# Kernel tuning notes

Measured on AMD Instinct MI355X. Metric: run time of the kernel, lower is better.

Reference implementation:

```python
import jax, jax.numpy as jnp
import numpy as np

CAPACITY = 0.5  # top_k = int(seq_len * capacity)

def setup_inputs() -> dict:
    key = jax.random.key(0)
    k1, k2, k3, k4 = jax.random.split(key, 4)
    b, s, d, d_ff = 4, 4096, 1024, 4096
    x = jax.random.normal(k1, (b, s, d), dtype=jnp.float32)
    mask = jnp.ones((b, s), dtype=jnp.bool_)
    # learned params: router (Linear(d,1,bias=False)) and the block MLP
    Wr = jax.random.normal(k2, (d, 1), dtype=jnp.float32) * (d ** -0.5)
    W1 = jax.random.normal(k3, (d, d_ff), dtype=jnp.float32) * (d ** -0.5)
    W2 = jax.random.normal(k4, (d_ff, d), dtype=jnp.float32) * (d_ff ** -0.5)
    return {"x": x, "mask": mask, "Wr": Wr, "W1": W1, "W2": W2}

def reference(x, mask, Wr, W1, W2):
    b, s, d = x.shape
    top_k = int(s * CAPACITY)
    # router logits [b, s]
    logits = (x @ Wr)[..., 0]
    # top-k over sequence dim (torch sorted=False; softmax/gather are
    # permutation-equivariant so sorted top_k gives identical results)
    vals, idx = jax.lax.top_k(logits, top_k)          # [b, k]
    order = jnp.argsort(idx, axis=1)                  # sort selected indices ascending
    sel = jnp.take_along_axis(idx, order, axis=1)     # [b, k] token positions, ascending
    w = jax.nn.softmax(vals, axis=1)                  # softmax over selected logits
    r_w = jnp.take_along_axis(w, order, axis=1)       # weights reordered to match sel
    # gather selected tokens
    fx = jnp.take_along_axis(x, sel[..., None], axis=1)  # [b, k, d]
    # block: residual MLP whose update is scaled by router weights (mask unused by MLP)
    h = jax.nn.silu(fx @ W1) @ W2
    out = fx + h * r_w[..., None]
    # scatter processed tokens back into x
    batch = jnp.arange(b)[:, None]
    hidden_states = x.at[batch, sel].set(out)
    # aux loss: faithful to the original (flat view + flat index set, then BCE-with-logits mean)
    flat_logits = logits.reshape(-1)                  # [b*s]
    targets = jnp.zeros_like(flat_logits).at[sel.reshape(-1)].set(1.0)
    aux_loss = jnp.mean(
        jnp.maximum(flat_logits, 0.0)
        - flat_logits * targets
        + jnp.log1p(jnp.exp(-jnp.abs(flat_logits)))
    )
    return hidden_states, aux_loss
```

## Files before the change

kernel.cpp:

```cpp
#include <hip/hip_runtime.h>
#include <hip/hip_bf16.h>
#include <cstdint>

#define B_ 4
#define S_ 4096
#define D_ 1024
#define DFF_ 4096
#define KSEL_ 2048
#define M_ (B_ * KSEL_)
#define NTOK_ (B_ * S_)

typedef short bf16x8 __attribute__((ext_vector_type(8)));
typedef float f32x4 __attribute__((ext_vector_type(4)));

__device__ inline unsigned short f2bf(float f) {
    union { float f; unsigned int u; } c; c.f = f;
    unsigned int u = c.u;
    unsigned int r = u + 0x7fffu + ((u >> 16) & 1u);
    return (unsigned short)(r >> 16);
}

__global__ __launch_bounds__(256)
void transpose_both(const float* __restrict__ W1, unsigned short* __restrict__ W1T,
                    const float* __restrict__ W2, unsigned short* __restrict__ W2T) {
    __shared__ float tile[32][33];
    const float* src; unsigned short* dst; int R, C, c0, r0;
    if (blockIdx.z == 0) { src = W1; dst = W1T; R = D_;  C = DFF_;
                           c0 = blockIdx.x * 32; r0 = blockIdx.y * 32; }
    else                 { src = W2; dst = W2T; R = DFF_; C = D_;
                           c0 = blockIdx.y * 32; r0 = blockIdx.x * 32; }
    for (int i = threadIdx.y; i < 32; i += 8)
        tile[i][threadIdx.x] = src[(size_t)(r0 + i) * C + c0 + threadIdx.x];
    __syncthreads();
    for (int i = threadIdx.y; i < 32; i += 8)
        dst[(size_t)(c0 + i) * R + r0 + threadIdx.x] = f2bf(tile[threadIdx.x][i]);
}

__global__ __launch_bounds__(256)
void router_kernel(const float* __restrict__ x, const float* __restrict__ Wr,
                   float* __restrict__ logits, unsigned short* __restrict__ xb,
                   float* __restrict__ out) {
    int wid = threadIdx.x >> 6, lane = threadIdx.x & 63;
    int row = blockIdx.x * 4 + wid;
    const float* xr = x + (size_t)row * D_;
    unsigned short* xbr = xb + (size_t)row * D_;
    float* outr = out + (size_t)row * D_;
    float acc = 0.f;
#pragma unroll
    for (int j = 0; j < 4; j++) {
        int off = j * 256 + lane * 4;
        float4 v = *(const float4*)(xr + off);
        float4 w = *(const float4*)(Wr + off);
        acc += v.x * w.x + v.y * w.y + v.z * w.z + v.w * w.w;
        *(float4*)(outr + off) = v;
        ushort4 o;
        o.x = f2bf(v.x); o.y = f2bf(v.y); o.z = f2bf(v.z); o.w = f2bf(v.w);
        *(ushort4*)(xbr + off) = o;
    }
#pragma unroll
    for (int s = 32; s; s >>= 1) acc += __shfl_xor(acc, s);
    if (lane == 0) logits[row] = acc;
}

__global__ __launch_bounds__(256)
void rank_partial_kernel(const float* __restrict__ logits, int* __restrict__ rank) {
    __shared__ float lj[512];
    int b  = blockIdx.x >> 7;
    int ic = (blockIdx.x >> 3) & 15;
    int jc = blockIdx.x & 7;
    const float* L = logits + b * S_;
    for (int t = threadIdx.x; t < 512; t += 256) lj[t] = L[jc * 512 + t];
    __syncthreads();
    int i = ic * 256 + threadIdx.x;
    float li = L[i];
    int jbase = jc * 512;
    int r = 0;
    const float4* __restrict__ lj4 = (const float4*)lj;
#pragma unroll 4
    for (int q = 0; q < 128; q++) {
        float4 v = lj4[q];
        int jb = jbase + q * 4;
        r += (v.x > li) | ((v.x == li) & (jb     < i));
        r += (v.y > li) | ((v.y == li) & (jb + 1 < i));
        r += (v.z > li) | ((v.z == li) & (jb + 2 < i));
        r += (v.w > li) | ((v.w == li) & (jb + 3 < i));
    }
    atomicAdd(&rank[b * S_ + i], r);
}

__global__ __launch_bounds__(256)
void compact_kernel(const float* __restrict__ logits, const int* __restrict__ rank,
                    int* __restrict__ rowidx, float* __restrict__ rw) {
    __shared__ float lg[S_];
    __shared__ int f[S_];
    __shared__ int tsum[256];
    __shared__ float red[256];
    int b = blockIdx.x;
    const float* L = logits + b * S_;
    const int* R = rank + b * S_;
    for (int j = threadIdx.x; j < S_ / 4; j += 256) {
        ((float4*)lg)[j] = ((const float4*)L)[j];
        int4 rk = ((const int4*)R)[j];
        int4 fl;
        fl.x = rk.x < KSEL_; fl.y = rk.y < KSEL_;
        fl.z = rk.z < KSEL_; fl.w = rk.w < KSEL_;
        ((int4*)f)[j] = fl;
    }
    __syncthreads();
    float mx = -INFINITY;
    for (int j = threadIdx.x; j < S_; j += 256) mx = fmaxf(mx, lg[j]);
    red[threadIdx.x] = mx; __syncthreads();
    for (int s = 128; s; s >>= 1) {
        if (threadIdx.x < s) red[threadIdx.x] = fmaxf(red[threadIdx.x], red[threadIdx.x + s]);
        __syncthreads();
    }
    float m = red[0];
    __syncthreads();

    float esum = 0.f;
    int s0 = 0;
#pragma unroll
    for (int j = 0; j < 16; j++) {
        int i = threadIdx.x * 16 + j;
        s0 += f[i];
        if (f[i]) esum += expf(lg[i] - m);
    }
    red[threadIdx.x] = esum; __syncthreads();
    for (int s = 128; s; s >>= 1) {
        if (threadIdx.x < s) red[threadIdx.x] += red[threadIdx.x + s];
        __syncthreads();
    }
    float inv = 1.f / red[0];

    tsum[threadIdx.x] = s0; __syncthreads();
    for (int s = 1; s < 256; s <<= 1) {
        int u = (threadIdx.x >= s) ? tsum[threadIdx.x - s] : 0;
        __syncthreads();
        tsum[threadIdx.x] += u;
        __syncthreads();
    }
    int pos = tsum[threadIdx.x] - s0;
    for (int j = 0; j < 16; j++) {
        int i = threadIdx.x * 16 + j;
        if (f[i]) {
            rowidx[b * KSEL_ + pos] = b * S_ + i;
            rw[b * KSEL_ + pos] = expf(lg[i] - m) * inv;
            pos++;
        }
    }
}

__global__ __launch_bounds__(256)
void loss_kernel(const float* __restrict__ logits, const int* __restrict__ rank,
                 float* __restrict__ partials) {
    __shared__ float red[256];
    int i = blockIdx.x * 256 + threadIdx.x;
    float l = logits[i];
    float t = 0.f;
    if (i < S_)
        t = ((rank[i] < KSEL_) | (rank[S_ + i] < KSEL_) |
             (rank[2 * S_ + i] < KSEL_) | (rank[3 * S_ + i] < KSEL_)) ? 1.f : 0.f;
    float v = fmaxf(l, 0.f) - l * t + log1pf(expf(-fabsf(l)));
    red[threadIdx.x] = v; __syncthreads();
    for (int s = 128; s; s >>= 1) {
        if (threadIdx.x < s) red[threadIdx.x] += red[threadIdx.x + s];
        __syncthreads();
    }
    if (threadIdx.x == 0) partials[blockIdx.x] = red[0];
}

__global__ void loss_final(const float* __restrict__ partials, float* __restrict__ out) {
    float v = partials[threadIdx.x];
#pragma unroll
    for (int s = 32; s; s >>= 1) v += __shfl_xor(v, s);
    if (threadIdx.x == 0) out[0] = v / (float)NTOK_;
}

template <int MODE>
__global__ __launch_bounds__(256)
void gemm_bt_kernel(const unsigned short* __restrict__ A,
                    const unsigned short* __restrict__ BT,
                    const int* __restrict__ rowidx,
                    const float* __restrict__ rw,
                    const float* __restrict__ x,
                    unsigned short* __restrict__ Hout,
                    float* __restrict__ Out,
                    int K, int N) {
    __shared__ __attribute__((aligned(16))) unsigned short As[128 * 64];
    __shared__ __attribute__((aligned(16))) unsigned short Bs[128 * 64];
    __shared__ __attribute__((aligned(16))) float Cs[32 * 132];
    const int tid = threadIdx.x;
    const int w = tid >> 6, lane = tid & 63;
    const int wm = w >> 1, wn = w & 1;
    const int tile_m = blockIdx.x * 128;
    const int tile_n = blockIdx.y * 128;

    const int srow = lane >> 3;
    const int sw = (lane & 7) ^ srow;
    const uint64_t abase = (uint64_t)(uintptr_t)A;
    const uint64_t bbase = (uint64_t)(uintptr_t)BT;
    uint64_t aaddr[4], baddr[4];
#pragma unroll
    for (int t = 0; t < 4; ++t) {
        int r = t * 32 + w * 8 + srow;
        int am = tile_m + r;
        int ar = (MODE == 1) ? rowidx[am] : am;
        aaddr[t] = abase + ((uint64_t)ar * K + (uint64_t)sw * 8) * 2ull;
        int bn = tile_n + r;
        baddr[t] = bbase + ((uint64_t)bn * K + (uint64_t)sw * 8) * 2ull;
    }

    f32x4 acc[4][4];
#pragma unroll
    for (int i = 0; i < 4; i++)
#pragma unroll
        for (int j = 0; j < 4; j++) acc[i][j] = (f32x4){0.f, 0.f, 0.f, 0.f};

    const int lr = lane & 15, quad = lane >> 4;
    const int KI = K >> 6;
    for (int it = 0; it < KI; ++it) {
        const uint64_t koff = (uint64_t)(it * 64) * 2ull;
#pragma unroll
        for (int t = 0; t < 4; ++t) {
            unsigned short* ldsA = &As[(t * 32 + w * 8) * 64];
            unsigned short* ldsB = &Bs[(t * 32 + w * 8) * 64];
            __builtin_amdgcn_global_load_lds(
                (const __attribute__((address_space(1))) unsigned int*)(uintptr_t)(aaddr[t] + koff),
                (__attribute__((address_space(3))) unsigned int*)ldsA, 16, 0, 0);
            __builtin_amdgcn_global_load_lds(
                (const __attribute__((address_space(1))) unsigned int*)(uintptr_t)(baddr[t] + koff),
                (__attribute__((address_space(3))) unsigned int*)ldsB, 16, 0, 0);
        }
        __syncthreads();
#pragma unroll
        for (int ks = 0; ks < 2; ++ks) {
            bf16x8 af[4], bfr[4];
#pragma unroll
            for (int t4 = 0; t4 < 4; ++t4) {
                int row = wm * 64 + t4 * 16 + lr;
                int kc = ks * 4 + quad;
                af[t4] = *(const bf16x8*)((const char*)As + row * 128 + ((kc ^ (lr & 7)) * 16));
                int nr = wn * 64 + t4 * 16 + lr;
                bfr[t4] = *(const bf16x8*)((const char*)Bs + nr * 128 + ((kc ^ (lr & 7)) * 16));
            }
#pragma unroll
            for (int ti = 0; ti < 4; ++ti)
#pragma unroll
                for (int tj = 0; tj < 4; ++tj)
                    acc[ti][tj] = __builtin_amdgcn_mfma_f32_16x16x32_bf16(
                        af[ti], bfr[tj], acc[ti][tj], 0, 0, 0);
        }
        __syncthreads();
    }

    const int erow = tid >> 3;
    const int eseg = tid & 7;
#pragma unroll
    for (int p = 0; p < 4; ++p) {
        if (p) __syncthreads();
        if (wm == (p >> 1)) {
#pragma unroll
            for (int t = 0; t < 2; ++t) {
                int ti = (p & 1) * 2 + t;
#pragma unroll
                for (int tj = 0; tj < 4; ++tj) {
                    int rbase = t * 16 + quad * 4;
                    int col = wn * 64 + tj * 16 + lr;
#pragma unroll
                    for (int r = 0; r < 4; ++r)
                        Cs[(rbase + r) * 132 + col] = acc[ti][tj][r];
                }
            }
        }
        __syncthreads();
        int m = tile_m + p * 32 + erow;
        const float* crow = Cs + erow * 132 + eseg * 16;
        if (MODE == 1) {
            uint64_t hb = (uint64_t)m * N + tile_n + eseg * 16;
#pragma unroll
            for (int c = 0; c < 2; ++c) {
                f32x4 v0 = *(const f32x4*)(crow + c * 8);
                f32x4 v1 = *(const f32x4*)(crow + c * 8 + 4);
                float s[8];
#pragma unroll
                for (int j = 0; j < 4; ++j) {
                    s[j]     = v0[j] * __builtin_amdgcn_rcpf(1.f + __expf(-v0[j]));
                    s[4 + j] = v1[j] * __builtin_amdgcn_rcpf(1.f + __expf(-v1[j]));
                }
                union { __hip_bfloat162 h; unsigned int u; } cv;
                uint4 pk;
                cv.h = __float22bfloat162_rn(float2{s[0], s[1]}); pk.x = cv.u;
                cv.h = __float22bfloat162_rn(float2{s[2], s[3]}); pk.y = cv.u;
                cv.h = __float22bfloat162_rn(float2{s[4], s[5]}); pk.z = cv.u;
                cv.h = __float22bfloat162_rn(float2{s[6], s[7]}); pk.w = cv.u;
                *(uint4*)(Hout + hb + c * 8) = pk;
            }
        } else {
            int grow = rowidx[m];
            float wgt = rw[m];
            uint64_t gb = (uint64_t)grow * D_ + tile_n + eseg * 16;
#pragma unroll
            for (int c = 0; c < 4; ++c) {
                f32x4 v = *(const f32x4*)(crow + c * 4);
                float4 xv = *(const float4*)(x + gb + c * 4);
                float4 o;
                o.x = xv.x + v[0] * wgt;
                o.y = xv.y + v[1] * wgt;
                o.z = xv.z + v[2] * wgt;
                o.w = xv.w + v[3] * wgt;
                *(float4*)(Out + gb + c * 4) = o;
            }
        }
    }
}

extern "C" void kernel_launch(void* const* d_in, const int* in_sizes, int n_in,
                              void* d_out, int out_size, void* d_ws, size_t ws_size,
                              hipStream_t stream) {
    const float* x  = (const float*)d_in[0];
    const float* Wr = (const float*)d_in[2];
    const float* W1 = (const float*)d_in[3];
    const float* W2 = (const float*)d_in[4];
    float* out = (float*)d_out;

    char* ws = (char*)d_ws;
    size_t off = 0;
    auto alloc = [&](size_t bytes) {
        char* p = ws + off;
        off = (off + bytes + 255) & ~(size_t)255;
        return p;
    };
    unsigned short* xb   = (unsigned short*)alloc((size_t)NTOK_ * D_ * 2);
    unsigned short* W1bT = (unsigned short*)alloc((size_t)DFF_ * D_ * 2);
    unsigned short* W2bT = (unsigned short*)alloc((size_t)D_ * DFF_ * 2);
    unsigned short* H    = (unsigned short*)alloc((size_t)M_ * DFF_ * 2);
    float* logits  = (float*)alloc(NTOK_ * 4);
    int*   rank    = (int*)alloc(NTOK_ * 4);
    int*   rowidx  = (int*)alloc(M_ * 4);
    float* rwp     = (float*)alloc(M_ * 4);
    float* partials = (float*)alloc(64 * 4);

    (void)hipMemsetAsync(rank, 0, NTOK_ * 4, stream);

    transpose_both<<<dim3(128, 32, 2), dim3(32, 8), 0, stream>>>(W1, W1bT, W2, W2bT);
    router_kernel<<<NTOK_ / 4, 256, 0, stream>>>(x, Wr, logits, xb, out);
    rank_partial_kernel<<<512, 256, 0, stream>>>(logits, rank);
    compact_kernel<<<B_, 256, 0, stream>>>(logits, rank, rowidx, rwp);
    loss_kernel<<<NTOK_ / 256, 256, 0, stream>>>(logits, rank, partials);
    loss_final<<<1, 64, 0, stream>>>(partials, out + (size_t)NTOK_ * D_);
    gemm_bt_kernel<1><<<dim3(M_ / 128, DFF_ / 128), 256, 0, stream>>>(
        xb, W1bT, rowidx, nullptr, nullptr, H, nullptr, D_, DFF_);
    gemm_bt_kernel<2><<<dim3(M_ / 128, D_ / 128), 256, 0, stream>>>(
        H, W2bT, rowidx, rwp, x, nullptr, out, DFF_, D_);
}
```

Baseline: 372.0 us.

## Split GEMM kernels, use 64-row tiles for second GEMM, copy only unselected rows

The templated GEMM is split into two kernels. The second GEMM now uses 64x128 tiles, which doubles its block count from 512 to 1024 so more CUs stay busy on the small N=1024 output. The router kernel no longer writes all of x to the output. A new kernel copies only the unselected rows after ranking, which halves the redundant output write traffic. The cost is an extra kernel launch and less operand reuse per block in the second GEMM.

```diff
diff --git a/kernel.cpp b/kernel.cpp
--- a/kernel.cpp
+++ b/kernel.cpp
@@ -38,13 +38,11 @@
 
 __global__ __launch_bounds__(256)
 void router_kernel(const float* __restrict__ x, const float* __restrict__ Wr,
-                   float* __restrict__ logits, unsigned short* __restrict__ xb,
-                   float* __restrict__ out) {
+                   float* __restrict__ logits, unsigned short* __restrict__ xb) {
     int wid = threadIdx.x >> 6, lane = threadIdx.x & 63;
     int row = blockIdx.x * 4 + wid;
     const float* xr = x + (size_t)row * D_;
     unsigned short* xbr = xb + (size_t)row * D_;
-    float* outr = out + (size_t)row * D_;
     float acc = 0.f;
 #pragma unroll
     for (int j = 0; j < 4; j++) {
@@ -52,7 +50,6 @@
         float4 v = *(const float4*)(xr + off);
         float4 w = *(const float4*)(Wr + off);
         acc += v.x * w.x + v.y * w.y + v.z * w.z + v.w * w.w;
-        *(float4*)(outr + off) = v;
         ushort4 o;
         o.x = f2bf(v.x); o.y = f2bf(v.y); o.z = f2bf(v.z); o.w = f2bf(v.w);
         *(ushort4*)(xbr + off) = o;
@@ -89,6 +86,16 @@
 }
 
 __global__ __launch_bounds__(256)
+void copy_unselected_kernel(const float* __restrict__ x, const int* __restrict__ rank,
+                            float* __restrict__ out) {
+    int row = blockIdx.x;
+    if (rank[row] < KSEL_) return;
+    const float4* src = (const float4*)(x + (size_t)row * D_);
+    float4* dst = (float4*)(out + (size_t)row * D_);
+    dst[threadIdx.x] = src[threadIdx.x];
+}
+
+__global__ __launch_bounds__(256)
 void compact_kernel(const float* __restrict__ logits, const int* __restrict__ rank,
                     int* __restrict__ rowidx, float* __restrict__ rw) {
     __shared__ float lg[S_];
@@ -176,16 +183,12 @@
     if (threadIdx.x == 0) out[0] = v / (float)NTOK_;
 }
 
-template <int MODE>
-__global__ __launch_bounds__(256)
-void gemm_bt_kernel(const unsigned short* __restrict__ A,
-                    const unsigned short* __restrict__ BT,
-                    const int* __restrict__ rowidx,
-                    const float* __restrict__ rw,
-                    const float* __restrict__ x,
-                    unsigned short* __restrict__ Hout,
-                    float* __restrict__ Out,
-                    int K, int N) {
+__global__ __launch_bounds__(256)
+void gemm1_kernel(const unsigned short* __restrict__ A,
+                  const unsigned short* __restrict__ BT,
+                  const int* __restrict__ rowidx,
+                  unsigned short* __restrict__ Hout,
+                  int K, int N) {
     __shared__ __attribute__((aligned(16))) unsigned short As[128 * 64];
     __shared__ __attribute__((aligned(16))) unsigned short Bs[128 * 64];
     __shared__ __attribute__((aligned(16))) float Cs[32 * 132];
@@ -203,8 +206,7 @@
 #pragma unroll
     for (int t = 0; t < 4; ++t) {
         int r = t * 32 + w * 8 + srow;
-        int am = tile_m + r;
-        int ar = (MODE == 1) ? rowidx[am] : am;
+        int ar = rowidx[tile_m + r];
         aaddr[t] = abase + ((uint64_t)ar * K + (uint64_t)sw * 8) * 2ull;
         int bn = tile_n + r;
         baddr[t] = bbase + ((uint64_t)bn * K + (uint64_t)sw * 8) * 2ull;
@@ -253,8 +255,7 @@
         __syncthreads();
     }
 
-    const int erow = tid >> 3;
-    const int eseg = tid & 7;
+    const int erow = tid >> 3, eseg = tid & 7;
 #pragma unroll
     for (int p = 0; p < 4; ++p) {
         if (p) __syncthreads();
@@ -275,41 +276,137 @@
         __syncthreads();
         int m = tile_m + p * 32 + erow;
         const float* crow = Cs + erow * 132 + eseg * 16;
-        if (MODE == 1) {
-            uint64_t hb = (uint64_t)m * N + tile_n + eseg * 16;
-#pragma unroll
-            for (int c = 0; c < 2; ++c) {
-                f32x4 v0 = *(const f32x4*)(crow + c * 8);
-                f32x4 v1 = *(const f32x4*)(crow + c * 8 + 4);
-                float s[8];
-#pragma unroll
-                for (int j = 0; j < 4; ++j) {
-                    s[j]     = v0[j] * __builtin_amdgcn_rcpf(1.f + __expf(-v0[j]));
-                    s[4 + j] = v1[j] * __builtin_amdgcn_rcpf(1.f + __expf(-v1[j]));
-                }
-                union { __hip_bfloat162 h; unsigned int u; } cv;
-                uint4 pk;
-                cv.h = __float22bfloat162_rn(float2{s[0], s[1]}); pk.x = cv.u;
-                cv.h = __float22bfloat162_rn(float2{s[2], s[3]}); pk.y = cv.u;
-                cv.h = __float22bfloat162_rn(float2{s[4], s[5]}); pk.z = cv.u;
-                cv.h = __float22bfloat162_rn(float2{s[6], s[7]}); pk.w = cv.u;
-                *(uint4*)(Hout + hb + c * 8) = pk;
+        uint64_t hb = (uint64_t)m * N + tile_n + eseg * 16;
+#pragma unroll
+        for (int c = 0; c < 2; ++c) {
+            f32x4 v0 = *(const f32x4*)(crow + c * 8);
+            f32x4 v1 = *(const f32x4*)(crow + c * 8 + 4);
+            float s[8];
+#pragma unroll
+            for (int j = 0; j < 4; ++j) {
+                s[j]     = v0[j] * __builtin_amdgcn_rcpf(1.f + __expf(-v0[j]));
+                s[4 + j] = v1[j] * __builtin_amdgcn_rcpf(1.f + __expf(-v1[j]));
             }
-        } else {
-            int grow = rowidx[m];
-            float wgt = rw[m];
-            uint64_t gb = (uint64_t)grow * D_ + tile_n + eseg * 16;
-#pragma unroll
-            for (int c = 0; c < 4; ++c) {
-                f32x4 v = *(const f32x4*)(crow + c * 4);
-                float4 xv = *(const float4*)(x + gb + c * 4);
-                float4 o;
-                o.x = xv.x + v[0] * wgt;
-                o.y = xv.y + v[1] * wgt;
-                o.z = xv.z + v[2] * wgt;
-                o.w = xv.w + v[3] * wgt;
-                *(float4*)(Out + gb + c * 4) = o;
+            union { __hip_bfloat162 h; unsigned int u; } cv;
+            uint4 pk;
+            cv.h = __float22bfloat162_rn(float2{s[0], s[1]}); pk.x = cv.u;
+            cv.h = __float22bfloat162_rn(float2{s[2], s[3]}); pk.y = cv.u;
+            cv.h = __float22bfloat162_rn(float2{s[4], s[5]}); pk.z = cv.u;
+            cv.h = __float22bfloat162_rn(float2{s[6], s[7]}); pk.w = cv.u;
+            *(uint4*)(Hout + hb + c * 8) = pk;
+        }
+    }
+}
+
+__global__ __launch_bounds__(256)
+void gemm2_kernel(const unsigned short* __restrict__ A,
+                  const unsigned short* __restrict__ BT,
+                  const int* __restrict__ rowidx,
+                  const float* __restrict__ rw,
+                  const float* __restrict__ x,
+                  float* __restrict__ Out,
+                  int K, int N) {
+    __shared__ __attribute__((aligned(16))) unsigned short As[64 * 64];
+    __shared__ __attribute__((aligned(16))) unsigned short Bs[128 * 64];
+    __shared__ __attribute__((aligned(16))) float Cs[16 * 132];
+    const int tid = threadIdx.x;
+    const int w = tid >> 6, lane = tid & 63;
+    const int tile_m = blockIdx.x * 64;
+    const int tile_n = blockIdx.y * 128;
+
+    const int srow = lane >> 3;
+    const int sw = (lane & 7) ^ srow;
+    const uint64_t abase = (uint64_t)(uintptr_t)A;
+    const uint64_t bbase = (uint64_t)(uintptr_t)BT;
+    uint64_t aaddr[2], baddr[4];
+#pragma unroll
+    for (int t = 0; t < 2; ++t) {
+        int r = t * 32 + w * 8 + srow;
+        aaddr[t] = abase + ((uint64_t)(tile_m + r) * K + (uint64_t)sw * 8) * 2ull;
+    }
+#pragma unroll
+    for (int t = 0; t < 4; ++t) {
+        int bn = tile_n + t * 32 + w * 8 + srow;
+        baddr[t] = bbase + ((uint64_t)bn * K + (uint64_t)sw * 8) * 2ull;
+    }
+
+    f32x4 acc[4][2];
+#pragma unroll
+    for (int i = 0; i < 4; i++)
+#pragma unroll
+        for (int j = 0; j < 2; j++) acc[i][j] = (f32x4){0.f, 0.f, 0.f, 0.f};
+
+    const int lr = lane & 15, quad = lane >> 4;
+    const int KI = K >> 6;
+    for (int it = 0; it < KI; ++it) {
+        const uint64_t koff = (uint64_t)(it * 64) * 2ull;
+#pragma unroll
+        for (int t = 0; t < 2; ++t) {
+            unsigned short* ldsA = &As[(t * 32 + w * 8) * 64];
+            __builtin_amdgcn_global_load_lds(
+                (const __attribute__((address_space(1))) unsigned int*)(uintptr_t)(aaddr[t] + koff),
+                (__attribute__((address_space(3))) unsigned int*)ldsA, 16, 0, 0);
+        }
+#pragma unroll
+        for (int t = 0; t < 4; ++t) {
+            unsigned short* ldsB = &Bs[(t * 32 + w * 8) * 64];
+            __builtin_amdgcn_global_load_lds(
+                (const __attribute__((address_space(1))) unsigned int*)(uintptr_t)(baddr[t] + koff),
+                (__attribute__((address_space(3))) unsigned int*)ldsB, 16, 0, 0);
+        }
+        __syncthreads();
+#pragma unroll
+        for (int ks = 0; ks < 2; ++ks) {
+            bf16x8 af[4], bfr[2];
+            int kc = ks * 4 + quad;
+#pragma unroll
+            for (int t4 = 0; t4 < 4; ++t4) {
+                int row = t4 * 16 + lr;
+                af[t4] = *(const bf16x8*)((const char*)As + row * 128 + ((kc ^ (lr & 7)) * 16));
             }
+#pragma unroll
+            for (int t2 = 0; t2 < 2; ++t2) {
+                int nr = w * 32 + t2 * 16 + lr;
+                bfr[t2] = *(const bf16x8*)((const char*)Bs + nr * 128 + ((kc ^ (lr & 7)) * 16));
+            }
+#pragma unroll
+            for (int ti = 0; ti < 4; ++ti)
+#pragma unroll
+                for (int tj = 0; tj < 2; ++tj)
+                    acc[ti][tj] = __builtin_amdgcn_mfma_f32_16x16x32_bf16(
+                        af[ti], bfr[tj], acc[ti][tj], 0, 0, 0);
+        }
+        __syncthreads();
+    }
+
+    const int erow = tid >> 4;
+    const int eseg = tid & 15;
+#pragma unroll
+    for (int p = 0; p < 4; ++p) {
+        if (p) __syncthreads();
+#pragma unroll
+        for (int tj = 0; tj < 2; ++tj) {
+            int col = w * 32 + tj * 16 + lr;
+#pragma unroll
+            for (int r = 0; r < 4; ++r)
+                Cs[(quad * 4 + r) * 132 + col] = acc[p][tj][r];
+        }
+        __syncthreads();
+        int m = tile_m + p * 16 + erow;
+        int grow = rowidx[m];
+        float wgt = rw[m];
+        const float* crow = Cs + erow * 132 + eseg * 8;
+        uint64_t gb = (uint64_t)grow * D_ + tile_n + eseg * 8;
+#pragma unroll
+        for (int c = 0; c < 2; ++c) {
+            f32x4 v = *(const f32x4*)(crow + c * 4);
+            float4 xv = *(const float4*)(x + gb + c * 4);
+            float4 o;
+            o.x = xv.x + v[0] * wgt;
+            o.y = xv.y + v[1] * wgt;
+            o.z = xv.z + v[2] * wgt;
+            o.w = xv.w + v[3] * wgt;
+            *(float4*)(Out + gb + c * 4) = o;
         }
     }
 }
@@ -343,13 +440,14 @@
     (void)hipMemsetAsync(rank, 0, NTOK_ * 4, stream);
 
     transpose_both<<<dim3(128, 32, 2), dim3(32, 8), 0, stream>>>(W1, W1bT, W2, W2bT);
-    router_kernel<<<NTOK_ / 4, 256, 0, stream>>>(x, Wr, logits, xb, out);
+    router_kernel<<<NTOK_ / 4, 256, 0, stream>>>(x, Wr, logits, xb);
     rank_partial_kernel<<<512, 256, 0, stream>>>(logits, rank);
+    copy_unselected_kernel<<<NTOK_, 256, 0, stream>>>(x, rank, out);
     compact_kernel<<<B_, 256, 0, stream>>>(logits, rank, rowidx, rwp);
     loss_kernel<<<NTOK_ / 256, 256, 0, stream>>>(logits, rank, partials);
     loss_final<<<1, 64, 0, stream>>>(partials, out + (size_t)NTOK_ * D_);
-    gemm_bt_kernel<1><<<dim3(M_ / 128, DFF_ / 128), 256, 0, stream>>>(
-        xb, W1bT, rowidx, nullptr, nullptr, H, nullptr, D_, DFF_);
-    gemm_bt_kernel<2><<<dim3(M_ / 128, D_ / 128), 256, 0, stream>>>(
-        H, W2bT, rowidx, rwp, x, nullptr, out, DFF_, D_);
-}
+    gemm1_kernel<<<dim3(M_ / 128, DFF_ / 128), 256, 0, stream>>>(
+        xb, W1bT, rowidx, H, D_, DFF_);
+    gemm2_kernel<<<dim3(M_ / 64, D_ / 128), 256, 0, stream>>>(
+        H, W2bT, rowidx, rwp, x, out, DFF_, D_);
+}
```

Result: slower. 384.1 us (+3.2%).

## Merge prep kernels and fuse rank/compact/loss into one cooperative kernel

Applied to the files above, without the earlier changes.

The weight transpose and router/cast kernels become a single launch that branches on block index. The rank, compaction, softmax and aux-loss kernels become one cooperative kernel that uses grid-wide syncs, a ballot-based compaction and atomic accumulation of the softmax sum and loss. This removes several small launches and the single-block-per-batch compact step. The softmax now uses exp(l) without subtracting the max, which risks overflow for large logits. The float atomics also make the summation order nondeterministic.

```diff
diff --git a/kernel.cpp b/kernel.cpp
--- a/kernel.cpp
+++ b/kernel.cpp
@@ -1,6 +1,9 @@
 #include <hip/hip_runtime.h>
 #include <hip/hip_bf16.h>
+#include <hip/hip_cooperative_groups.h>
 #include <cstdint>
+
+namespace cg = cooperative_groups;
 
 #define B_ 4
 #define S_ 4096
@@ -21,61 +24,81 @@
 }
 
 __global__ __launch_bounds__(256)
-void transpose_both(const float* __restrict__ W1, unsigned short* __restrict__ W1T,
-                    const float* __restrict__ W2, unsigned short* __restrict__ W2T) {
+void prep_kernel(const float* __restrict__ W1, unsigned short* __restrict__ W1T,
+                 const float* __restrict__ W2, unsigned short* __restrict__ W2T,
+                 const float* __restrict__ x, const float* __restrict__ Wr,
+                 float* __restrict__ logits, unsigned short* __restrict__ xb,
+                 float* __restrict__ out) {
     __shared__ float tile[32][33];
-    const float* src; unsigned short* dst; int R, C, c0, r0;
-    if (blockIdx.z == 0) { src = W1; dst = W1T; R = D_;  C = DFF_;
-                           c0 = blockIdx.x * 32; r0 = blockIdx.y * 32; }
-    else                 { src = W2; dst = W2T; R = DFF_; C = D_;
-                           c0 = blockIdx.y * 32; r0 = blockIdx.x * 32; }
-    for (int i = threadIdx.y; i < 32; i += 8)
-        tile[i][threadIdx.x] = src[(size_t)(r0 + i) * C + c0 + threadIdx.x];
+    const int blk = blockIdx.x;
+    const int tid = threadIdx.x;
+    if (blk < 8192) {
+        const float* src; unsigned short* dst; int R, C, c0, r0;
+        if (blk < 4096) {
+            int bx = blk & 127, by = blk >> 7;
+            src = W1; dst = W1T; R = D_; C = DFF_;
+            c0 = bx * 32; r0 = by * 32;
+        } else {
+            int t = blk - 4096;
+            int bx = t & 127, by = t >> 7;
+            src = W2; dst = W2T; R = DFF_; C = D_;
+            c0 = by * 32; r0 = bx * 32;
+        }
+        int tx = tid & 31, ty = tid >> 5;
+        for (int i = ty; i < 32; i += 8)
+            tile[i][tx] = src[(size_t)(r0 + i) * C + c0 + tx];
+        __syncthreads();
+        for (int i = ty; i < 32; i += 8)
+            dst[(size_t)(c0 + i) * R + r0 + tx] = f2bf(tile[tx][i]);
+    } else {
+        int rb = blk - 8192;
+        int wid = tid >> 6, lane = tid & 63;
+        int row = rb * 4 + wid;
+        const float* xr = x + (size_t)row * D_;
+        unsigned short* xbr = xb + (size_t)row * D_;
+        float* outr = out + (size_t)row * D_;
+        float acc = 0.f;
+#pragma unroll
+        for (int j = 0; j < 4; j++) {
+            int off = j * 256 + lane * 4;
+            float4 v = *(const float4*)(xr + off);
+            float4 w = *(const float4*)(Wr + off);
+            acc += v.x * w.x + v.y * w.y + v.z * w.z + v.w * w.w;
+            *(float4*)(outr + off) = v;
+            ushort4 o;
+            o.x = f2bf(v.x); o.y = f2bf(v.y); o.z = f2bf(v.z); o.w = f2bf(v.w);
+            *(ushort4*)(xbr + off) = o;
+        }
+#pragma unroll
+        for (int s = 32; s; s >>= 1) acc += __shfl_xor(acc, s);
+        if (lane == 0) logits[row] = acc;
+    }
+}
+
+__global__ __launch_bounds__(256)
+void select_coop(const float* __restrict__ logits, int* __restrict__ rank,
+                 float* __restrict__ bsum, int* __restrict__ segcnt,
+                 int* __restrict__ rowidx, float* __restrict__ rw,
+                 float* __restrict__ lossout) {
+    cg::grid_group grid = cg::this_grid();
+    __shared__ float lj[512];
+    __shared__ float redf[256];
+    __shared__ int redi[4];
+    const int tid = threadIdx.x;
+    const int blk = blockIdx.x;
+    const int b  = blk >> 7;
+    const int ic = (blk >> 3) & 15;
+    const int jc = blk & 7;
+    const float* L = logits + b * S_;
+
+    if (blk == 0 && tid < 4) bsum[tid] = 0.f;
+    for (int t = tid; t < 512; t += 256) lj[t] = L[jc * 512 + t];
     __syncthreads();
-    for (int i = threadIdx.y; i < 32; i += 8)
-        dst[(size_t)(c0 + i) * R + r0 + threadIdx.x] = f2bf(tile[threadIdx.x][i]);
-}
-
-__global__ __launch_bounds__(256)
-void router_kernel(const float* __restrict__ x, const float* __restrict__ Wr,
-                   float* __restrict__ logits, unsigned short* __restrict__ xb,
-                   float* __restrict__ out) {
-    int wid = threadIdx.x >> 6, lane = threadIdx.x & 63;
-    int row = blockIdx.x * 4 + wid;
-    const float* xr = x + (size_t)row * D_;
-    unsigned short* xbr = xb + (size_t)row * D_;
-    float* outr = out + (size_t)row * D_;
-    float acc = 0.f;
-#pragma unroll
-    for (int j = 0; j < 4; j++) {
-        int off = j * 256 + lane * 4;
-        float4 v = *(const float4*)(xr + off);
-        float4 w = *(const float4*)(Wr + off);
-        acc += v.x * w.x + v.y * w.y + v.z * w.z + v.w * w.w;
-        *(float4*)(outr + off) = v;
-        ushort4 o;
-        o.x = f2bf(v.x); o.y = f2bf(v.y); o.z = f2bf(v.z); o.w = f2bf(v.w);
-        *(ushort4*)(xbr + off) = o;
-    }
-#pragma unroll
-    for (int s = 32; s; s >>= 1) acc += __shfl_xor(acc, s);
-    if (lane == 0) logits[row] = acc;
-}
-
-__global__ __launch_bounds__(256)
-void rank_partial_kernel(const float* __restrict__ logits, int* __restrict__ rank) {
-    __shared__ float lj[512];
-    int b  = blockIdx.x >> 7;
-    int ic = (blockIdx.x >> 3) & 15;
-    int jc = blockIdx.x & 7;
-    const float* L = logits + b * S_;
-    for (int t = threadIdx.x; t < 512; t += 256) lj[t] = L[jc * 512 + t];
-    __syncthreads();
-    int i = ic * 256 + threadIdx.x;
-    float li = L[i];
-    int jbase = jc * 512;
+    const int i = ic * 256 + tid;
+    const float li = L[i];
+    const int jbase = jc * 512;
     int r = 0;
-    const float4* __restrict__ lj4 = (const float4*)lj;
+    const float4* lj4 = (const float4*)lj;
 #pragma unroll 4
     for (int q = 0; q < 128; q++) {
         float4 v = lj4[q];
@@ -86,94 +109,58 @@
         r += (v.w > li) | ((v.w == li) & (jb + 3 < i));
     }
     atomicAdd(&rank[b * S_ + i], r);
-}
-
-__global__ __launch_bounds__(256)
-void compact_kernel(const float* __restrict__ logits, const int* __restrict__ rank,
-                    int* __restrict__ rowidx, float* __restrict__ rw) {
-    __shared__ float lg[S_];
-    __shared__ int f[S_];
-    __shared__ int tsum[256];
-    __shared__ float red[256];
-    int b = blockIdx.x;
-    const float* L = logits + b * S_;
-    const int* R = rank + b * S_;
-    for (int j = threadIdx.x; j < S_ / 4; j += 256) {
-        ((float4*)lg)[j] = ((const float4*)L)[j];
-        int4 rk = ((const int4*)R)[j];
-        int4 fl;
-        fl.x = rk.x < KSEL_; fl.y = rk.y < KSEL_;
-        fl.z = rk.z < KSEL_; fl.w = rk.w < KSEL_;
-        ((int4*)f)[j] = fl;
-    }
-    __syncthreads();
-    float mx = -INFINITY;
-    for (int j = threadIdx.x; j < S_; j += 256) mx = fmaxf(mx, lg[j]);
-    red[threadIdx.x] = mx; __syncthreads();
-    for (int s = 128; s; s >>= 1) {
-        if (threadIdx.x < s) red[threadIdx.x] = fmaxf(red[threadIdx.x], red[threadIdx.x + s]);
-        __syncthreads();
-    }
-    float m = red[0];
-    __syncthreads();
-
-    float esum = 0.f;
-    int s0 = 0;
-#pragma unroll
-    for (int j = 0; j < 16; j++) {
-        int i = threadIdx.x * 16 + j;
-        s0 += f[i];
-        if (f[i]) esum += expf(lg[i] - m);
-    }
-    red[threadIdx.x] = esum; __syncthreads();
-    for (int s = 128; s; s >>= 1) {
-        if (threadIdx.x < s) red[threadIdx.x] += red[threadIdx.x + s];
-        __syncthreads();
-    }
-    float inv = 1.f / red[0];
-
-    tsum[threadIdx.x] = s0; __syncthreads();
-    for (int s = 1; s < 256; s <<= 1) {
-        int u = (threadIdx.x >= s) ? tsum[threadIdx.x - s] : 0;
-        __syncthreads();
-        tsum[threadIdx.x] += u;
-        __syncthreads();
-    }
-    int pos = tsum[threadIdx.x] - s0;
-    for (int j = 0; j < 16; j++) {
-        int i = threadIdx.x * 16 + j;
-        if (f[i]) {
+
+    grid.sync();
+
+    int sel = 0;
+    float e = 0.f;
+    const int lane = tid & 63, wv = tid >> 6;
+    if (jc == 0) {
+        sel = rank[b * S_ + i] < KSEL_;
+        e = sel ? __expf(li) : 0.f;
+        redf[tid] = e; __syncthreads();
+        for (int s = 128; s; s >>= 1) {
+            if (tid < s) redf[tid] += redf[tid + s];
+            __syncthreads();
+        }
+        if (tid == 0) atomicAdd(&bsum[b], redf[0]);
+        unsigned long long mask = __ballot(sel);
+        if (lane == 0) redi[wv] = __popcll(mask);
+        __syncthreads();
+        if (tid == 0) segcnt[b * 16 + ic] = redi[0] + redi[1] + redi[2] + redi[3];
+        if (b == 0 && ic == 0 && tid == 0) lossout[0] = 0.f;
+    }
+
+    grid.sync();
+
+    if (jc == 0) {
+        int segoff = 0;
+        for (int k = 0; k < ic; k++) segoff += segcnt[b * 16 + k];
+        unsigned long long mask = __ballot(sel);
+        if (lane == 0) redi[wv] = __popcll(mask);
+        __syncthreads();
+        int woff = 0;
+        for (int k = 0; k < wv; k++) woff += redi[k];
+        int before = __popcll(mask & ((1ull << lane) - 1ull));
+        if (sel) {
+            int pos = segoff + woff + before;
             rowidx[b * KSEL_ + pos] = b * S_ + i;
-            rw[b * KSEL_ + pos] = expf(lg[i] - m) * inv;
-            pos++;
-        }
-    }
-}
-
-__global__ __launch_bounds__(256)
-void loss_kernel(const float* __restrict__ logits, const int* __restrict__ rank,
-                 float* __restrict__ partials) {
-    __shared__ float red[256];
-    int i = blockIdx.x * 256 + threadIdx.x;
-    float l = logits[i];
-    float t = 0.f;
-    if (i < S_)
-        t = ((rank[i] < KSEL_) | (rank[S_ + i] < KSEL_) |
-             (rank[2 * S_ + i] < KSEL_) | (rank[3 * S_ + i] < KSEL_)) ? 1.f : 0.f;
-    float v = fmaxf(l, 0.f) - l * t + log1pf(expf(-fabsf(l)));
-    red[threadIdx.x] = v; __syncthreads();
-    for (int s = 128; s; s >>= 1) {
-        if (threadIdx.x < s) red[threadIdx.x] += red[threadIdx.x + s];
-        __syncthreads();
-    }
-    if (threadIdx.x == 0) partials[blockIdx.x] = red[0];
-}
-
-__global__ void loss_final(const float* __restrict__ partials, float* __restrict__ out) {
-    float v = partials[threadIdx.x];
-#pragma unroll
-    for (int s = 32; s; s >>= 1) v += __shfl_xor(v, s);
-    if (threadIdx.x == 0) out[0] = v / (float)NTOK_;
+            rw[b * KSEL_ + pos] = e / bsum[b];
+        }
+        int fi = (b * 16 + ic) * 256 + tid;
+        float l = logits[fi];
+        float t = 0.f;
+        if (fi < S_)
+            t = ((rank[fi] < KSEL_) | (rank[S_ + fi] < KSEL_) |
+                 (rank[2 * S_ + fi] < KSEL_) | (rank[3 * S_ + fi] < KSEL_)) ? 1.f : 0.f;
+        float v = fmaxf(l, 0.f) - l * t + log1pf(expf(-fabsf(l)));
+        redf[tid] = v; __syncthreads();
+        for (int s = 128; s; s >>= 1) {
+            if (tid < s) redf[tid] += redf[tid + s];
+            __syncthreads();
+        }
+        if (tid == 0) atomicAdd(lossout, redf[0] * (1.f / (float)NTOK_));
+    }
 }
 
 template <int MODE>
@@ -253,8 +240,7 @@
         __syncthreads();
     }
 
-    const int erow = tid >> 3;
-    const int eseg = tid & 7;
+    const int erow = tid >> 3, eseg = tid & 7;
 #pragma unroll
     for (int p = 0; p < 4; ++p) {
         if (p) __syncthreads();
@@ -338,16 +324,21 @@
     int*   rank    = (int*)alloc(NTOK_ * 4);
     int*   rowidx  = (int*)alloc(M_ * 4);
     float* rwp     = (float*)alloc(M_ * 4);
-    float* partials = (float*)alloc(64 * 4);
+    float* bsum    = (float*)alloc(4 * 4);
+    int*   segcnt  = (int*)alloc(64 * 4);
+    float* lossptr = out + (size_t)NTOK_ * D_;
 
     (void)hipMemsetAsync(rank, 0, NTOK_ * 4, stream);
 
-    transpose_both<<<dim3(128, 32, 2), dim3(32, 8), 0, stream>>>(W1, W1bT, W2, W2bT);
-    router_kernel<<<NTOK_ / 4, 256, 0, stream>>>(x, Wr, logits, xb, out);
-    rank_partial_kernel<<<512, 256, 0, stream>>>(logits, rank);
-    compact_kernel<<<B_, 256, 0, stream>>>(logits, rank, rowidx, rwp);
-    loss_kernel<<<NTOK_ / 256, 256, 0, stream>>>(logits, rank, partials);
-    loss_final<<<1, 64, 0, stream>>>(partials, out + (size_t)NTOK_ * D_);
+    prep_kernel<<<12288, 256, 0, stream>>>(W1, W1bT, W2, W2bT, x, Wr, logits, xb, out);
+
+    {
+        void* args[] = {(void*)&logits, (void*)&rank, (void*)&bsum, (void*)&segcnt,
+                        (void*)&rowidx, (void*)&rwp, (void*)&lossptr};
+        (void)hipLaunchCooperativeKernel((void*)select_coop, dim3(512), dim3(256),
+                                         args, 0, stream);
+    }
+
     gemm_bt_kernel<1><<<dim3(M_ / 128, DFF_ / 128), 256, 0, stream>>>(
         xb, W1bT, rowidx, nullptr, nullptr, H, nullptr, D_, DFF_);
     gemm_bt_kernel<2><<<dim3(M_ / 128, D_ / 128), 256, 0, stream>>>(
```

Result: slower. 459.6 us (+23.5%).
